# Kernel tuning notes

Measured on AMD Instinct MI355X. Metric: run time of the kernel, lower is better.

The kernel has to match this reference:

```python
import jax, jax.numpy as jnp
import numpy as np

N_NODES = 50000
N_EDGES = 800000


def gat_conv(x, src, dst, ea, W, We, a_s, a_d, a_e, b, n_nodes):
    """PyG GATConv with edge_dim, add_self_loops=True, fill_value='mean', concat=True."""
    H, C = a_s.shape
    dt = x.dtype
    # self-loop edge_attr = mean of incoming edge attrs per destination node
    deg = jax.ops.segment_sum(jnp.ones((src.shape[0],), dt), dst, num_segments=n_nodes)
    loop_attr = jax.ops.segment_sum(ea, dst, num_segments=n_nodes) / jnp.clip(deg, 1.0)[:, None]
    nodes = jnp.arange(n_nodes, dtype=src.dtype)
    s = jnp.concatenate([src, nodes])
    d = jnp.concatenate([dst, nodes])
    e_attr = jnp.concatenate([ea, loop_attr], axis=0)       # [E2, edge_dim]
    h = (x @ W).reshape(n_nodes, H, C)                       # [N,H,C]
    e = (e_attr @ We).reshape(-1, H, C)                      # [E2,H,C]
    a_src = jnp.einsum('nhc,hc->nh', h, a_s)                 # [N,H]
    a_dst = jnp.einsum('nhc,hc->nh', h, a_d)
    a_edg = jnp.einsum('ehc,hc->eh', e, a_e)                 # [E2,H]
    lg = jax.nn.leaky_relu(a_src[s] + a_dst[d] + a_edg, 0.2)  # [E2,H]
    m = jax.ops.segment_max(lg, d, num_segments=n_nodes)     # every node has a self-loop
    p = jnp.exp(lg - m[d])
    z = jax.ops.segment_sum(p, d, num_segments=n_nodes)
    alpha = p / z[d]                                         # segment softmax over dst
    out = jax.ops.segment_sum(alpha[:, :, None] * h[s], d, num_segments=n_nodes)
    return out.reshape(n_nodes, H * C) + b


def setup_inputs() -> dict:
    key = jax.random.key(0)
    ks = iter(jax.random.split(key, 40))
    sc = 0.05
    inp = {
        'x': jax.random.normal(next(ks), (N_NODES, 128), jnp.float32),
        'edge_index': jax.random.randint(next(ks), (2, N_EDGES), 0, N_NODES, dtype=jnp.int32),
        'edge_attr': jax.random.uniform(next(ks), (N_EDGES, 1), jnp.float32),
        'fa_w': jax.random.normal(next(ks), (128, 128)) * sc, 'fa_b': jnp.zeros((128,)),
        'W1': jax.random.normal(next(ks), (128, 256)) * sc, 'We1': jax.random.normal(next(ks), (1, 256)) * sc,
        'as1': jax.random.normal(next(ks), (4, 64)) * sc, 'ad1': jax.random.normal(next(ks), (4, 64)) * sc,
        'ae1': jax.random.normal(next(ks), (4, 64)) * sc, 'b1': jnp.zeros((256,)),
        'W2': jax.random.normal(next(ks), (256, 256)) * sc, 'We2': jax.random.normal(next(ks), (1, 256)) * sc,
        'as2': jax.random.normal(next(ks), (4, 64)) * sc, 'ad2': jax.random.normal(next(ks), (4, 64)) * sc,
        'ae2': jax.random.normal(next(ks), (4, 64)) * sc, 'b2': jnp.zeros((256,)),
        'W3': jax.random.normal(next(ks), (256, 64)) * sc, 'We3': jax.random.normal(next(ks), (1, 64)) * sc,
        'as3': jax.random.normal(next(ks), (1, 64)) * sc, 'ad3': jax.random.normal(next(ks), (1, 64)) * sc,
        'ae3': jax.random.normal(next(ks), (1, 64)) * sc, 'b3': jnp.zeros((64,)),
        'r1_w': jax.random.normal(next(ks), (128, 256)) * sc, 'r1_b': jnp.zeros((256,)),
        'r2_w': jax.random.normal(next(ks), (256, 256)) * sc, 'r2_b': jnp.zeros((256,)),
        'ffn_w1': jax.random.normal(next(ks), (128, 64)) * sc, 'ffn_b1': jnp.zeros((64,)),
        'ffn_w2': jax.random.normal(next(ks), (64, 64)) * sc, 'ffn_b2': jnp.zeros((64,)),
    }
    return inp


def reference(x, edge_index, edge_attr, fa_w, fa_b,
              W1, We1, as1, ad1, ae1, b1,
              W2, We2, as2, ad2, ae2, b2,
              W3, We3, as3, ad3, ae3, b3,
              r1_w, r1_b, r2_w, r2_b,
              ffn_w1, ffn_b1, ffn_w2, ffn_b2):
    n = x.shape[0]
    src, dst = edge_index[0], edge_index[1]
    # feature attention gate
    x = x * jax.nn.sigmoid(x @ fa_w + fa_b)
    xr1 = x @ r1_w + r1_b
    z1 = gat_conv(x, src, dst, edge_attr, W1, We1, as1, ad1, ae1, b1, n)
    z1 = jax.nn.leaky_relu(z1, 0.01) + xr1          # dropout = identity (eval)
    z2 = gat_conv(z1, src, dst, edge_attr, W2, We2, as2, ad2, ae2, b2, n)
    z2 = jax.nn.leaky_relu(z2, 0.01) + (z1 @ r2_w + r2_b)
    z3 = gat_conv(z2, src, dst, edge_attr, W3, We3, as3, ad3, ae3, b3, n)
    z_self = jax.nn.relu(x @ ffn_w1 + ffn_b1) @ ffn_w2 + ffn_b2
    z3 = jax.nn.leaky_relu(z3, 0.01) + z_self
    return z3
```

## Files before the change

### kernel.cpp

```cpp
#include <hip/hip_runtime.h>
#include <hip/hip_bf16.h>


typedef unsigned short u16;
typedef unsigned int   u32;
typedef __attribute__((ext_vector_type(8))) short short8;
typedef __attribute__((ext_vector_type(4))) float float4v;

typedef const __attribute__((address_space(1))) u32* gptr_t;
typedef __attribute__((address_space(3))) u32* lptr_t;
#define GLOAD_LDS16(g, l) \
    __builtin_amdgcn_global_load_lds((gptr_t)(const void*)(g), (lptr_t)(void*)(l), 16, 0, 0)

static __device__ __forceinline__ u16 f2b(float f) {
    u32 u = __float_as_uint(f);
    u32 r = u + 0x7fffu + ((u >> 16) & 1u);
    return (u16)(r >> 16);
}
static __device__ __forceinline__ float b2f(u16 u) {
    return __uint_as_float(((u32)u) << 16);
}
static __device__ __forceinline__ float lo2f(u32 v) { return __uint_as_float(v << 16); }
static __device__ __forceinline__ float hi2f(u32 v) { return __uint_as_float(v & 0xffff0000u); }
static __device__ __forceinline__ float lrelu02(float x) { return fmaxf(x, 0.2f * x); }

__global__ void prep_mega(const float* __restrict__ x, u16* __restrict__ xb, int n4,
                          const float* s0, const float* s1, const float* s2,
                          const float* s3, const float* s4, const float* s5,
                          const float* s6, const float* s7,
                          u16* d0, u16* d1, u16* d2, u16* d3,
                          u16* d4, u16* d5, u16* d6, u16* d7,
                          const float* We1, const float* ae1,
                          const float* We2, const float* ae2,
                          const float* We3, const float* ae3, float* ce_g,
                          const int* __restrict__ ei,
                          u32* deg, u32* rank, int E) {
    int role = blockIdx.y;
    if (role == 0) {
        int i = blockIdx.x * 256 + threadIdx.x;
        if (i >= n4) return;
        float4 v = ((const float4*)x)[i];
        ushort4 o;
        o.x = f2b(v.x); o.y = f2b(v.y); o.z = f2b(v.z); o.w = f2b(v.w);
        ((ushort4*)xb)[i] = o;
    } else if (role == 2) {
        int e = blockIdx.x * 256 + threadIdx.x;
        if (e >= E) return;
        int d = ei[E + e];
        rank[e] = atomicAdd(&deg[d], 1u);
    } else {
        int wid = blockIdx.x >> 4, sub = blockIdx.x & 15;
        if (wid > 8) return;
        if (wid == 8) {
            if (sub == 0) {
                int t = threadIdx.x;
                if (t < 9) {
                    const float* W; const float* a; int h;
                    if (t < 4)      { W = We1; a = ae1; h = t; }
                    else if (t < 8) { W = We2; a = ae2; h = t - 4; }
                    else            { W = We3; a = ae3; h = 0; }
                    float s = 0.f;
                    for (int c = 0; c < 64; c++) s += W[h * 64 + c] * a[h * 64 + c];
                    ce_g[t] = s;
                }
            }
            return;
        }
        const float* src; u16* dst; int K, N;
        switch (wid) {
            case 0: src = s0; dst = d0; K = 128; N = 128; break;
            case 1: src = s1; dst = d1; K = 128; N = 256; break;
            case 2: src = s2; dst = d2; K = 128; N = 256; break;
            case 3: src = s3; dst = d3; K = 256; N = 256; break;
            case 4: src = s4; dst = d4; K = 256; N = 256; break;
            case 5: src = s5; dst = d5; K = 256; N = 64;  break;
            case 6: src = s6; dst = d6; K = 128; N = 64;  break;
            default: src = s7; dst = d7; K = 64;  N = 64;  break;
        }
        int KN = K * N;
        int nmask = N - 1;
        int nshift = __popc((u32)nmask);
        for (int i = sub * 256 + threadIdx.x; i < KN; i += 16 * 256) {
            int k = i >> nshift, n2 = i & nmask;
            dst[(size_t)n2 * K + k] = f2b(src[i]);
        }
    }
}

__global__ void scan_block_kernel(const u32* __restrict__ deg, int* incl,
                                  int* blocksum, int Nn) {
    __shared__ int sb[256];
    int t = threadIdx.x;
    int n = blockIdx.x * 256 + t;
    int v = (n < Nn) ? (int)deg[n] : 0;
    sb[t] = v;
    __syncthreads();
    for (int off = 1; off < 256; off <<= 1) {
        int x = (t >= off) ? sb[t - off] : 0;
        __syncthreads();
        sb[t] += x;
        __syncthreads();
    }
    if (n < Nn) incl[n] = sb[t];
    if (t == 255) blocksum[blockIdx.x] = sb[255];
}

__global__ void scan_final_kernel(const u32* __restrict__ deg, const int* __restrict__ incl,
                                  const int* __restrict__ blocksum,
                                  int* row_ptr, int Nn) {
    __shared__ int sb[256];
    int t = threadIdx.x;
    int b = blockIdx.x;
    sb[t] = (t < b) ? blocksum[t] : 0;
    __syncthreads();
    for (int off = 128; off > 0; off >>= 1) {
        if (t < off) sb[t] += sb[t + off];
        __syncthreads();
    }
    int base = sb[0];
    int n = b * 256 + t;
    if (n >= Nn) return;
    int d = (int)deg[n];
    int excl = base + incl[n] - d;
    row_ptr[n] = excl;
    if (n == Nn - 1) row_ptr[Nn] = excl + d;
}

__global__ void scatter_kernel(const int* __restrict__ ei, const float* __restrict__ ea,
                               const int* __restrict__ row_ptr, const u32* __restrict__ rank,
                               int2* __restrict__ csr2, int E) {
    int e = blockIdx.x * 256 + threadIdx.x;
    if (e >= E) return;
    int d = ei[E + e];
    int pos = row_ptr[d] + (int)rank[e];
    csr2[pos] = make_int2(ei[e], __float_as_int(ea[e]));
}

template <int EPI, int K>
__global__ __launch_bounds__(256)
void gemm128_kernel(const u16* __restrict__ A, const u16* __restrict__ Bt,
                    const float* __restrict__ bias1, const float* __restrict__ bias2,
                    u16* __restrict__ Cres, u16* __restrict__ Ch, u16* __restrict__ Cmid) {
    __shared__ u16 As[128 * 32];
    __shared__ u16 Bs[128 * 32];
    int t = threadIdx.x;
    int w = t >> 6, lane = t & 63;
    int wm = w & 1, wn = w >> 1;
    int lm = lane & 15, q = lane >> 4;
    int bm = blockIdx.x * 128, bn = blockIdx.y * 128;

    float4v acc[4][4];
#pragma unroll
    for (int i = 0; i < 4; i++)
#pragma unroll
        for (int j = 0; j < 4; j++) acc[i][j] = (float4v){0.f, 0.f, 0.f, 0.f};

    int srow = lane >> 2;
    int scol = (lane & 3) * 8;
    const u16* aG = A + (size_t)(bm + w * 32 + srow) * K + scol;
    const u16* bG = Bt + (size_t)(bn + w * 32 + srow) * K + scol;
    u16* aL0 = &As[(w * 32) * 32];
    u16* aL1 = &As[(w * 32 + 16) * 32];
    u16* bL0 = &Bs[(w * 32) * 32];
    u16* bL1 = &Bs[(w * 32 + 16) * 32];

#pragma unroll
    for (int k0 = 0; k0 < K; k0 += 32) {
        GLOAD_LDS16(aG + k0, aL0);
        GLOAD_LDS16(aG + (size_t)16 * K + k0, aL1);
        GLOAD_LDS16(bG + k0, bL0);
        GLOAD_LDS16(bG + (size_t)16 * K + k0, bL1);
        __syncthreads();

        short8 af[4], bf[4];
#pragma unroll
        for (int i = 0; i < 4; i++)
            af[i] = *(const short8*)&As[(64 * wm + 16 * i + lm) * 32 + q * 8];
#pragma unroll
        for (int j = 0; j < 4; j++)
            bf[j] = *(const short8*)&Bs[(64 * wn + 16 * j + lm) * 32 + q * 8];
#pragma unroll
        for (int i = 0; i < 4; i++)
#pragma unroll
            for (int j = 0; j < 4; j++)
                acc[i][j] = __builtin_amdgcn_mfma_f32_16x16x32_bf16(af[i], bf[j], acc[i][j], 0, 0, 0);
        __syncthreads();
    }

#pragma unroll
    for (int i = 0; i < 4; i++)
#pragma unroll
        for (int j = 0; j < 4; j++) {
            int col = bn + 64 * wn + 16 * j + lm;
#pragma unroll
            for (int r = 0; r < 4; r++) {
                int row = bm + 64 * wm + 16 * i + q * 4 + r;
                float v = acc[i][j][r];
                if (col < 256) {
                    Cres[(size_t)row * 256 + col] = f2b(v + bias1[col]);
                } else if (EPI == 4 || col < 512) {
                    Ch[(size_t)row * 256 + (col - 256)] = f2b(v);
                } else if (col < 576) {
                    Cmid[(size_t)row * 64 + (col - 512)] = f2b(fmaxf(v + bias2[col - 512], 0.f));
                }
            }
        }
}

template <int EPI, int K>
__global__ __launch_bounds__(256)
void gemm_kernel(const u16* __restrict__ A, const u16* __restrict__ Bt,
                 const float* __restrict__ bias, const u16* __restrict__ extraB,
                 u16* __restrict__ Cb, int N) {
#define LDSS 40
    __shared__ u16 As[64 * LDSS];
    __shared__ u16 Bs[64 * LDSS];
    int t = threadIdx.x;
    int bm = blockIdx.x * 64, bn = blockIdx.y * 64;
    int w = t >> 6, lane = t & 63;
    int wm = w & 1, wn = w >> 1;
    int lm = lane & 15, q = lane >> 4;

    float4v acc[2][2];
#pragma unroll
    for (int i = 0; i < 2; i++)
#pragma unroll
        for (int j = 0; j < 2; j++) acc[i][j] = (float4v){0.f, 0.f, 0.f, 0.f};

    int ar = t >> 2;
    int ac = (t & 3) * 8;
    const u16* aPtr = A + (size_t)(bm + ar) * K + ac;
    const u16* bPtr = Bt + (size_t)(bn + ar) * K + ac;

#pragma unroll
    for (int k0 = 0; k0 < K; k0 += 32) {
        uint4 av = *(const uint4*)(aPtr + k0);
        uint4 bv = *(const uint4*)(bPtr + k0);
        *(uint4*)&As[ar * LDSS + ac] = av;
        *(uint4*)&Bs[ar * LDSS + ac] = bv;
        __syncthreads();

        short8 fa0 = *(const short8*)&As[(32 * wm + lm) * LDSS + q * 8];
        short8 fa1 = *(const short8*)&As[(32 * wm + 16 + lm) * LDSS + q * 8];
        short8 fb0 = *(const short8*)&Bs[(32 * wn + lm) * LDSS + q * 8];
        short8 fb1 = *(const short8*)&Bs[(32 * wn + 16 + lm) * LDSS + q * 8];
        acc[0][0] = __builtin_amdgcn_mfma_f32_16x16x32_bf16(fa0, fb0, acc[0][0], 0, 0, 0);
        acc[0][1] = __builtin_amdgcn_mfma_f32_16x16x32_bf16(fa0, fb1, acc[0][1], 0, 0, 0);
        acc[1][0] = __builtin_amdgcn_mfma_f32_16x16x32_bf16(fa1, fb0, acc[1][0], 0, 0, 0);
        acc[1][1] = __builtin_amdgcn_mfma_f32_16x16x32_bf16(fa1, fb1, acc[1][1], 0, 0, 0);
        __syncthreads();
    }

#pragma unroll
    for (int i = 0; i < 2; i++)
#pragma unroll
        for (int j = 0; j < 2; j++) {
            int col = bn + 32 * wn + 16 * j + lm;
            float bval = (EPI >= 1) ? bias[col] : 0.f;
#pragma unroll
            for (int r = 0; r < 4; r++) {
                int row = bm + 32 * wm + 16 * i + q * 4 + r;
                float v = acc[i][j][r] + bval;
                if (EPI == 3) {
                    float xv = b2f(extraB[(size_t)row * N + col]);
                    v = xv / (1.f + __expf(-v));
                }
                Cb[(size_t)row * N + col] = f2b(v);
            }
        }
}

__global__ __launch_bounds__(256)
void att4_kernel(const uint2* __restrict__ hb2, const float* __restrict__ a_s,
                 const float* __restrict__ a_d, float* att_s, float* att_d, int Nn) {
    int wv = threadIdx.x >> 6;
    int n = blockIdx.x * 4 + wv;
    if (n >= Nn) return;
    int lane = threadIdx.x & 63;
    float4 as4 = *(const float4*)&a_s[lane * 4];
    float4 ad4 = *(const float4*)&a_d[lane * 4];
    uint2 v = hb2[(size_t)n * 64 + lane];
    float c0 = lo2f(v.x), c1 = hi2f(v.x), c2 = lo2f(v.y), c3 = hi2f(v.y);
    float ps = c0 * as4.x + c1 * as4.y + c2 * as4.z + c3 * as4.w;
    float pd = c0 * ad4.x + c1 * ad4.y + c2 * ad4.z + c3 * ad4.w;
#pragma unroll
    for (int off = 8; off > 0; off >>= 1) {
        ps += __shfl_down(ps, off);
        pd += __shfl_down(pd, off);
    }
    if ((lane & 15) == 0) {
        att_s[n * 4 + (lane >> 4)] = ps;
        att_d[n * 4 + (lane >> 4)] = pd;
    }
}

__global__ __launch_bounds__(256)
void att1_kernel(const u32* __restrict__ hb, const float* __restrict__ a_s,
                 const float* __restrict__ a_d, float* att_s, float* att_d, int Nn) {
    int wv = threadIdx.x >> 6;
    int n = blockIdx.x * 4 + wv;
    if (n >= Nn) return;
    int lane = threadIdx.x & 63;
    int cl = lane & 31;
    float2 as2 = *(const float2*)&a_s[cl * 2];
    float2 ad2 = *(const float2*)&a_d[cl * 2];
    u32 v = hb[(u32)n * 32u + cl];
    float c0 = lo2f(v), c1 = hi2f(v);
    float ps = c0 * as2.x + c1 * as2.y;
    float pd = c0 * ad2.x + c1 * ad2.y;
    if (lane >= 32) { ps = 0.f; pd = 0.f; }
#pragma unroll
    for (int off = 16; off > 0; off >>= 1) {
        ps += __shfl_down(ps, off);
        pd += __shfl_down(pd, off);
    }
    if (lane == 0) {
        att_s[n] = ps;
        att_d[n] = pd;
    }
}

__global__ __launch_bounds__(256)
void agg4_kernel(const uint2* __restrict__ hb2,
                 const float* __restrict__ att_s, const float* __restrict__ att_d,
                 const int* __restrict__ row_ptr, const int2* __restrict__ csr2,
                 const float* __restrict__ ce_g, const float* __restrict__ bias,
                 const uint2* __restrict__ resid2, u16* __restrict__ outb, int Nn) {
    int wv = __builtin_amdgcn_readfirstlane(threadIdx.x >> 6);
    int n = blockIdx.x * 4 + wv;
    if (n >= Nn) return;
    int lane = threadIdx.x & 63;
    int hh = lane >> 4;

    float ce = ce_g[hh];
    float adn = att_d[n * 4 + hh];
    float asn = att_s[n * 4 + hh];
    uint2 sv = hb2[(size_t)n * 64 + lane];
    float z = 0.f, qsum = 0.f;
    float aA0 = 0.f, aA1 = 0.f, aA2 = 0.f, aA3 = 0.f;
    float aB0 = 0.f, aB1 = 0.f, aB2 = 0.f, aB3 = 0.f;

    int e0 = row_ptr[n], e1 = row_ptr[n + 1];
    for (int base = e0; base < e1; base += 64) {
        int cnt = min(64, e1 - base);
        int2 cc = csr2[base + min(lane, cnt - 1)];
        int vsrc = cc.x;
        float vea = __int_as_float(cc.y);
        int i = 0;
        for (; i + 4 <= cnt; i += 4) {
            int sA = __shfl(vsrc, i),     sB = __shfl(vsrc, i + 1);
            int sC = __shfl(vsrc, i + 2), sD = __shfl(vsrc, i + 3);
            float qA = __shfl(vea, i),     qB = __shfl(vea, i + 1);
            float qC = __shfl(vea, i + 2), qD = __shfl(vea, i + 3);
            float gA = att_s[(u32)sA * 4u + hh], gB = att_s[(u32)sB * 4u + hh];
            float gC = att_s[(u32)sC * 4u + hh], gD = att_s[(u32)sD * 4u + hh];
            uint2 vA = hb2[(u32)sA * 64u + lane], vB = hb2[(u32)sB * 64u + lane];
            uint2 vC = hb2[(u32)sC * 64u + lane], vD = hb2[(u32)sD * 64u + lane];
            float pA = __expf(lrelu02(gA + adn + qA * ce));
            float pB = __expf(lrelu02(gB + adn + qB * ce));
            float pC = __expf(lrelu02(gC + adn + qC * ce));
            float pD = __expf(lrelu02(gD + adn + qD * ce));
            qsum += (qA + qB) + (qC + qD);
            z += (pA + pB) + (pC + pD);
            aA0 = fmaf(pA, lo2f(vA.x), aA0); aA1 = fmaf(pA, hi2f(vA.x), aA1);
            aA2 = fmaf(pA, lo2f(vA.y), aA2); aA3 = fmaf(pA, hi2f(vA.y), aA3);
            aB0 = fmaf(pB, lo2f(vB.x), aB0); aB1 = fmaf(pB, hi2f(vB.x), aB1);
            aB2 = fmaf(pB, lo2f(vB.y), aB2); aB3 = fmaf(pB, hi2f(vB.y), aB3);
            aA0 = fmaf(pC, lo2f(vC.x), aA0); aA1 = fmaf(pC, hi2f(vC.x), aA1);
            aA2 = fmaf(pC, lo2f(vC.y), aA2); aA3 = fmaf(pC, hi2f(vC.y), aA3);
            aB0 = fmaf(pD, lo2f(vD.x), aB0); aB1 = fmaf(pD, hi2f(vD.x), aB1);
            aB2 = fmaf(pD, lo2f(vD.y), aB2); aB3 = fmaf(pD, hi2f(vD.y), aB3);
        }
        for (; i < cnt; i++) {
            int s = __shfl(vsrc, i);
            float q = __shfl(vea, i);
            float g = att_s[(u32)s * 4u + hh];
            uint2 v = hb2[(u32)s * 64u + lane];
            float p = __expf(lrelu02(g + adn + q * ce));
            qsum += q;
            z += p;
            aA0 = fmaf(p, lo2f(v.x), aA0); aA1 = fmaf(p, hi2f(v.x), aA1);
            aA2 = fmaf(p, lo2f(v.y), aA2); aA3 = fmaf(p, hi2f(v.y), aA3);
        }
    }
    float la = qsum / (float)max(e1 - e0, 1);
    float ps = __expf(lrelu02(asn + adn + la * ce));
    z += ps;
    float a0 = aA0 + aB0 + ps * lo2f(sv.x);
    float a1 = aA1 + aB1 + ps * hi2f(sv.x);
    float a2 = aA2 + aB2 + ps * lo2f(sv.y);
    float a3 = aA3 + aB3 + ps * hi2f(sv.y);

    float inv = 1.f / z;
    int c0 = lane * 4;
    float4 bv = *(const float4*)&bias[c0];
    uint2 rr = resid2[(size_t)n * 64 + lane];
    float o0 = fmaf(a0, inv, bv.x);
    float o1 = fmaf(a1, inv, bv.y);
    float o2 = fmaf(a2, inv, bv.z);
    float o3 = fmaf(a3, inv, bv.w);
    o0 = fmaxf(o0, 0.01f * o0) + lo2f(rr.x);
    o1 = fmaxf(o1, 0.01f * o1) + hi2f(rr.x);
    o2 = fmaxf(o2, 0.01f * o2) + lo2f(rr.y);
    o3 = fmaxf(o3, 0.01f * o3) + hi2f(rr.y);
    uint2 packed;
    packed.x = ((u32)f2b(o0)) | (((u32)f2b(o1)) << 16);
    packed.y = ((u32)f2b(o2)) | (((u32)f2b(o3)) << 16);
    ((uint2*)outb)[(size_t)n * 64 + lane] = packed;
}

__global__ __launch_bounds__(256)
void agg1_kernel(const uint2* __restrict__ hb2,
                 const float* __restrict__ att_s, const float* __restrict__ att_d,
                 const int* __restrict__ row_ptr, const int2* __restrict__ csr2,
                 const float* __restrict__ ce_g, const float* __restrict__ bias,
                 const uint2* __restrict__ zs2, float* __restrict__ outf, int Nn) {
    int wv = __builtin_amdgcn_readfirstlane(threadIdx.x >> 6);
    int n = blockIdx.x * 4 + wv;
    if (n >= Nn) return;
    int lane = threadIdx.x & 63;
    int qtr = lane >> 4;
    int cl = lane & 15;

    float ce = ce_g[8];
    float adn = att_d[n];
    float asn = att_s[n];
    uint2 sv = hb2[(u32)n * 16u + cl];
    float z = 0.f, qsum = 0.f;
    float a0 = 0.f, a1 = 0.f, a2 = 0.f, a3 = 0.f;

    int e0 = row_ptr[n], e1 = row_ptr[n + 1];
    for (int base = e0; base < e1; base += 64) {
        int cnt = min(64, e1 - base);
        int2 cc = csr2[base + min(lane, cnt - 1)];
        int vsrc = cc.x;
        float vea = __int_as_float(cc.y);
        for (int i = 0; i < cnt; i += 4) {
            int idx = min(i + qtr, cnt - 1);
            int s = __shfl(vsrc, idx);
            float q = __shfl(vea, idx);
            bool act = (i + qtr < cnt);
            float p = __expf(lrelu02(att_s[s] + adn + q * ce));
            p = act ? p : 0.f;
            q = act ? q : 0.f;
            uint2 v = hb2[(u32)s * 16u + cl];
            z += p;
            qsum += q;
            a0 = fmaf(p, lo2f(v.x), a0);
            a1 = fmaf(p, hi2f(v.x), a1);
            a2 = fmaf(p, lo2f(v.y), a2);
            a3 = fmaf(p, hi2f(v.y), a3);
        }
    }
    z += __shfl_xor(z, 16);       z += __shfl_xor(z, 32);
    qsum += __shfl_xor(qsum, 16); qsum += __shfl_xor(qsum, 32);
    a0 += __shfl_xor(a0, 16);     a0 += __shfl_xor(a0, 32);
    a1 += __shfl_xor(a1, 16);     a1 += __shfl_xor(a1, 32);
    a2 += __shfl_xor(a2, 16);     a2 += __shfl_xor(a2, 32);
    a3 += __shfl_xor(a3, 16);     a3 += __shfl_xor(a3, 32);

    float la = qsum / (float)max(e1 - e0, 1);
    float ps = __expf(lrelu02(asn + adn + la * ce));
    z += ps;
    a0 += ps * lo2f(sv.x);
    a1 += ps * hi2f(sv.x);
    a2 += ps * lo2f(sv.y);
    a3 += ps * hi2f(sv.y);

    if (lane < 16) {
        float inv = 1.f / z;
        int c0 = cl * 4;
        float4 bv = *(const float4*)&bias[c0];
        uint2 zz = zs2[(u32)n * 16u + cl];
        float o0 = fmaf(a0, inv, bv.x);
        float o1 = fmaf(a1, inv, bv.y);
        float o2 = fmaf(a2, inv, bv.z);
        float o3 = fmaf(a3, inv, bv.w);
        o0 = fmaxf(o0, 0.01f * o0) + lo2f(zz.x);
        o1 = fmaxf(o1, 0.01f * o1) + hi2f(zz.x);
        o2 = fmaxf(o2, 0.01f * o2) + lo2f(zz.y);
        o3 = fmaxf(o3, 0.01f * o3) + hi2f(zz.y);
        *(float4*)&outf[(size_t)n * 64 + c0] = make_float4(o0, o1, o2, o3);
    }
}

extern "C" void kernel_launch(void* const* d_in, const int* in_sizes, int n_in,
                              void* d_out, int out_size, void* d_ws, size_t ws_size,
                              hipStream_t stream) {
    const float* x    = (const float*)d_in[0];
    const int*   ei   = (const int*)d_in[1];
    const float* ea   = (const float*)d_in[2];
    const float* fa_w = (const float*)d_in[3];
    const float* fa_b = (const float*)d_in[4];
    const float* W1   = (const float*)d_in[5];
    const float* We1  = (const float*)d_in[6];
    const float* as1  = (const float*)d_in[7];
    const float* ad1  = (const float*)d_in[8];
    const float* ae1  = (const float*)d_in[9];
    const float* b1   = (const float*)d_in[10];
    const float* W2   = (const float*)d_in[11];
    const float* We2  = (const float*)d_in[12];
    const float* as2  = (const float*)d_in[13];
    const float* ad2  = (const float*)d_in[14];
    const float* ae2  = (const float*)d_in[15];
    const float* b2   = (const float*)d_in[16];
    const float* W3   = (const float*)d_in[17];
    const float* We3  = (const float*)d_in[18];
    const float* as3  = (const float*)d_in[19];
    const float* ad3  = (const float*)d_in[20];
    const float* ae3  = (const float*)d_in[21];
    const float* b3   = (const float*)d_in[22];
    const float* r1_w = (const float*)d_in[23];
    const float* r1_b = (const float*)d_in[24];
    const float* r2_w = (const float*)d_in[25];
    const float* r2_b = (const float*)d_in[26];
    const float* fw1  = (const float*)d_in[27];
    const float* fb1  = (const float*)d_in[28];
    const float* fw2  = (const float*)d_in[29];
    const float* fb2  = (const float*)d_in[30];

    const int Nn = in_sizes[0] / 128;
    const int E  = in_sizes[1] / 2;

    char* ws = (char*)d_ws;
    size_t off = 0;
    auto alloc = [&](size_t bytes) -> char* {
        char* p = ws + off;
        off += (bytes + 255) & ~((size_t)255);
        return p;
    };
    u32*   deg      = (u32*)alloc((size_t)Nn * 4);
    u32*   rank     = (u32*)alloc((size_t)E * 4);
    int*   incl     = (int*)alloc((size_t)Nn * 4);
    int*   row_ptr  = (int*)alloc((size_t)(Nn + 1) * 4);
    int*   blocksum = (int*)alloc(1024);
    float* att_s    = (float*)alloc((size_t)Nn * 16);
    float* att_d    = (float*)alloc((size_t)Nn * 16);
    int2*  csr2     = (int2*)alloc((size_t)E * 8);
    float* ce_g     = (float*)alloc(64);
    u16* xbf   = (u16*)alloc((size_t)(Nn + 128) * 128 * 2);
    u16* xg_bf = (u16*)alloc((size_t)(Nn + 128) * 128 * 2);
    u16* h_bf  = (u16*)alloc((size_t)(Nn + 128) * 256 * 2);
    u16* z_bf  = (u16*)alloc((size_t)(Nn + 128) * 256 * 2);
    u16* mid_bf = (u16*)alloc((size_t)(Nn + 128) * 64 * 2);
    u16* h3_bf  = (u16*)alloc((size_t)(Nn + 128) * 64 * 2);
    u16* wt_fa = (u16*)alloc(16384 * 2);
    u16* wt_c1 = (u16*)alloc((size_t)640 * 128 * 2);
    u16* wt_c2 = (u16*)alloc((size_t)512 * 256 * 2);
    u16* wt_W3 = (u16*)alloc(16384 * 2);
    u16* wt_f2 = (u16*)alloc(4096 * 2);
    u16* residB = (u16*)alloc((size_t)(Nn + 128) * 256 * 2);
    u16* zself  = (u16*)alloc((size_t)(Nn + 128) * 64 * 2);

    hipMemsetAsync(deg, 0, (size_t)Nn * 4, stream);

    int eb = (E + 255) / 256;
    int nb = (Nn + 255) / 256;
    int n4 = Nn * 128 / 4;
    int xb4 = (n4 + 255) / 256;

    prep_mega<<<dim3(max(xb4, eb), 3), 256, 0, stream>>>(
        x, xbf, n4,
        fa_w, r1_w, W1, r2_w, W2, W3, fw1, fw2,
        wt_fa, wt_c1, wt_c1 + (size_t)256 * 128, wt_c2, wt_c2 + (size_t)256 * 256,
        wt_W3, wt_c1 + (size_t)512 * 128, wt_f2, We1, ae1, We2, ae2, We3, ae3, ce_g,
        ei, deg, rank, E);
    scan_block_kernel<<<nb, 256, 0, stream>>>(deg, incl, blocksum, Nn);
    scan_final_kernel<<<nb, 256, 0, stream>>>(deg, incl, blocksum, row_ptr, Nn);
    scatter_kernel<<<eb, 256, 0, stream>>>(ei, ea, row_ptr, rank, csr2, E);

    int mb  = (Nn + 63) / 64;
    int mb1 = (Nn + 127) / 128;
    int ab  = (Nn + 3) / 4;

    gemm_kernel<3, 128><<<dim3(mb, 2), 256, 0, stream>>>(xbf, wt_fa, fa_b, xbf, xg_bf, 128);
    gemm128_kernel<6, 128><<<dim3(mb1, 5), 256, 0, stream>>>(xg_bf, wt_c1, r1_b, fb1,
                                                             residB, h_bf, mid_bf);
    att4_kernel<<<ab, 256, 0, stream>>>((const uint2*)h_bf, as1, ad1, att_s, att_d, Nn);
    agg4_kernel<<<ab, 256, 0, stream>>>((const uint2*)h_bf, att_s, att_d, row_ptr, csr2,
                                        ce_g, b1, (const uint2*)residB, z_bf, Nn);
    gemm128_kernel<4, 256><<<dim3(mb1, 4), 256, 0, stream>>>(z_bf, wt_c2, r2_b, nullptr,
                                                             residB, h_bf, nullptr);
    att4_kernel<<<ab, 256, 0, stream>>>((const uint2*)h_bf, as2, ad2, att_s, att_d, Nn);
    agg4_kernel<<<ab, 256, 0, stream>>>((const uint2*)h_bf, att_s, att_d, row_ptr, csr2,
                                        ce_g + 4, b2, (const uint2*)residB, z_bf, Nn);
    gemm_kernel<1, 64><<<dim3(mb, 1), 256, 0, stream>>>(mid_bf, wt_f2, fb2, nullptr, zself, 64);
    gemm_kernel<0, 256><<<dim3(mb, 1), 256, 0, stream>>>(z_bf, wt_W3, nullptr, nullptr, h3_bf, 64);
    att1_kernel<<<ab, 256, 0, stream>>>((const u32*)h3_bf, as3, ad3, att_s, att_d, Nn);
    agg1_kernel<<<ab, 256, 0, stream>>>((const uint2*)h3_bf, att_s, att_d, row_ptr, csr2,
                                        ce_g, b3, (const uint2*)zself, (float*)d_out, Nn);
}
```

Before: 494.8 us.

## Co-schedule CSR build with feature-gate and first combined GEMM

Moves the degree-counting atomics out of the prep kernel and into a merged launch alongside the feature-attention gate GEMM, using interleaved block roles. The CSR scatter is likewise merged into the first layer's combined GEMM launch, with one role in six doing a grid-stride scatter. This is meant to overlap the memory-bound graph preprocessing with compute-bound GEMMs and to drop a separate kernel launch. The trade-off is that the scatter and atomic roles use fewer blocks with grid-stride loops, which could lengthen the critical path if they finish after the GEMM blocks.

```diff
diff --git a/kernel.cpp b/kernel.cpp
--- a/kernel.cpp
+++ b/kernel.cpp
@@ -32,9 +32,7 @@
                           u16* d4, u16* d5, u16* d6, u16* d7,
                           const float* We1, const float* ae1,
                           const float* We2, const float* ae2,
-                          const float* We3, const float* ae3, float* ce_g,
-                          const int* __restrict__ ei,
-                          u32* deg, u32* rank, int E) {
+                          const float* We3, const float* ae3, float* ce_g) {
     int role = blockIdx.y;
     if (role == 0) {
         int i = blockIdx.x * 256 + threadIdx.x;
@@ -43,11 +41,6 @@
         ushort4 o;
         o.x = f2b(v.x); o.y = f2b(v.y); o.z = f2b(v.z); o.w = f2b(v.w);
         ((ushort4*)xb)[i] = o;
-    } else if (role == 2) {
-        int e = blockIdx.x * 256 + threadIdx.x;
-        if (e >= E) return;
-        int d = ei[E + e];
-        rank[e] = atomicAdd(&deg[d], 1u);
     } else {
         int wid = blockIdx.x >> 4, sub = blockIdx.x & 15;
         if (wid > 8) return;
@@ -126,28 +119,101 @@
     if (n == Nn - 1) row_ptr[Nn] = excl + d;
 }
 
-__global__ void scatter_kernel(const int* __restrict__ ei, const float* __restrict__ ea,
-                               const int* __restrict__ row_ptr, const u32* __restrict__ rank,
-                               int2* __restrict__ csr2, int E) {
-    int e = blockIdx.x * 256 + threadIdx.x;
-    if (e >= E) return;
-    int d = ei[E + e];
-    int pos = row_ptr[d] + (int)rank[e];
-    csr2[pos] = make_int2(ei[e], __float_as_int(ea[e]));
-}
-
-template <int EPI, int K>
+#define LDSS 40
 __global__ __launch_bounds__(256)
-void gemm128_kernel(const u16* __restrict__ A, const u16* __restrict__ Bt,
-                    const float* __restrict__ bias1, const float* __restrict__ bias2,
-                    u16* __restrict__ Cres, u16* __restrict__ Ch, u16* __restrict__ Cmid) {
+void fa_atomic_kernel(const u16* __restrict__ A, const u16* __restrict__ Bt,
+                      const float* __restrict__ bias, const u16* __restrict__ extraB,
+                      u16* __restrict__ Cb,
+                      const int* __restrict__ ei, u32* deg, u32* rank, int E, int nx) {
+    int gid = blockIdx.x;
+    int role = gid % 3;
+    int idx = gid / 3;
+    if (role == 2) {
+        for (int e = idx * 256 + threadIdx.x; e < E; e += nx * 256)
+            rank[e] = atomicAdd(&deg[ei[E + e]], 1u);
+        return;
+    }
+    __shared__ u16 As[64 * LDSS];
+    __shared__ u16 Bs[64 * LDSS];
+    const int K = 128, N = 128;
+    int t = threadIdx.x;
+    int bm = idx * 64, bn = role * 64;
+    int w = t >> 6, lane = t & 63;
+    int wm = w & 1, wn = w >> 1;
+    int lm = lane & 15, q = lane >> 4;
+
+    float4v acc[2][2];
+#pragma unroll
+    for (int i = 0; i < 2; i++)
+#pragma unroll
+        for (int j = 0; j < 2; j++) acc[i][j] = (float4v){0.f, 0.f, 0.f, 0.f};
+
+    int ar = t >> 2;
+    int ac = (t & 3) * 8;
+    const u16* aPtr = A + (size_t)(bm + ar) * K + ac;
+    const u16* bPtr = Bt + (size_t)(bn + ar) * K + ac;
+
+#pragma unroll
+    for (int k0 = 0; k0 < K; k0 += 32) {
+        uint4 av = *(const uint4*)(aPtr + k0);
+        uint4 bv = *(const uint4*)(bPtr + k0);
+        *(uint4*)&As[ar * LDSS + ac] = av;
+        *(uint4*)&Bs[ar * LDSS + ac] = bv;
+        __syncthreads();
+
+        short8 fa0 = *(const short8*)&As[(32 * wm + lm) * LDSS + q * 8];
+        short8 fa1 = *(const short8*)&As[(32 * wm + 16 + lm) * LDSS + q * 8];
+        short8 fb0 = *(const short8*)&Bs[(32 * wn + lm) * LDSS + q * 8];
+        short8 fb1 = *(const short8*)&Bs[(32 * wn + 16 + lm) * LDSS + q * 8];
+        acc[0][0] = __builtin_amdgcn_mfma_f32_16x16x32_bf16(fa0, fb0, acc[0][0], 0, 0, 0);
+        acc[0][1] = __builtin_amdgcn_mfma_f32_16x16x32_bf16(fa0, fb1, acc[0][1], 0, 0, 0);
+        acc[1][0] = __builtin_amdgcn_mfma_f32_16x16x32_bf16(fa1, fb0, acc[1][0], 0, 0, 0);
+        acc[1][1] = __builtin_amdgcn_mfma_f32_16x16x32_bf16(fa1, fb1, acc[1][1], 0, 0, 0);
+        __syncthreads();
+    }
+
+#pragma unroll
+    for (int i = 0; i < 2; i++)
+#pragma unroll
+        for (int j = 0; j < 2; j++) {
+            int col = bn + 32 * wn + 16 * j + lm;
+            float bval = bias[col];
+#pragma unroll
+            for (int r = 0; r < 4; r++) {
+                int row = bm + 32 * wm + 16 * i + q * 4 + r;
+                float v = acc[i][j][r] + bval;
+                float xv = b2f(extraB[(size_t)row * N + col]);
+                v = xv / (1.f + __expf(-v));
+                Cb[(size_t)row * N + col] = f2b(v);
+            }
+        }
+}
+
+__global__ __launch_bounds__(256)
+void c1_scatter_kernel(const u16* __restrict__ A, const u16* __restrict__ Bt,
+                       const float* __restrict__ bias1, const float* __restrict__ bias2,
+                       u16* __restrict__ Cres, u16* __restrict__ Ch, u16* __restrict__ Cmid,
+                       const int* __restrict__ ei, const float* __restrict__ ea,
+                       const int* __restrict__ row_ptr, const u32* __restrict__ rank,
+                       int2* __restrict__ csr2, int E, int nx) {
+    int gid = blockIdx.x;
+    int role = gid % 6;
+    int idx = gid / 6;
+    if (role == 5) {
+        for (int e = idx * 256 + threadIdx.x; e < E; e += nx * 256) {
+            int d = ei[E + e];
+            csr2[row_ptr[d] + (int)rank[e]] = make_int2(ei[e], __float_as_int(ea[e]));
+        }
+        return;
+    }
     __shared__ u16 As[128 * 32];
     __shared__ u16 Bs[128 * 32];
+    const int K = 128;
     int t = threadIdx.x;
     int w = t >> 6, lane = t & 63;
     int wm = w & 1, wn = w >> 1;
     int lm = lane & 15, q = lane >> 4;
-    int bm = blockIdx.x * 128, bn = blockIdx.y * 128;
+    int bm = idx * 128, bn = role * 128;
 
     float4v acc[4][4];
 #pragma unroll
@@ -198,7 +264,7 @@
                 float v = acc[i][j][r];
                 if (col < 256) {
                     Cres[(size_t)row * 256 + col] = f2b(v + bias1[col]);
-                } else if (EPI == 4 || col < 512) {
+                } else if (col < 512) {
                     Ch[(size_t)row * 256 + (col - 256)] = f2b(v);
                 } else if (col < 576) {
                     Cmid[(size_t)row * 64 + (col - 512)] = f2b(fmaxf(v + bias2[col - 512], 0.f));
@@ -207,12 +273,79 @@
         }
 }
 
+template <int K>
+__global__ __launch_bounds__(256)
+void gemm128_kernel(const u16* __restrict__ A, const u16* __restrict__ Bt,
+                    const float* __restrict__ bias1,
+                    u16* __restrict__ Cres, u16* __restrict__ Ch) {
+    __shared__ u16 As[128 * 32];
+    __shared__ u16 Bs[128 * 32];
+    int t = threadIdx.x;
+    int w = t >> 6, lane = t & 63;
+    int wm = w & 1, wn = w >> 1;
+    int lm = lane & 15, q = lane >> 4;
+    int bm = blockIdx.x * 128, bn = blockIdx.y * 128;
+
+    float4v acc[4][4];
+#pragma unroll
+    for (int i = 0; i < 4; i++)
+#pragma unroll
+        for (int j = 0; j < 4; j++) acc[i][j] = (float4v){0.f, 0.f, 0.f, 0.f};
+
+    int srow = lane >> 2;
+    int scol = (lane & 3) * 8;
+    const u16* aG = A + (size_t)(bm + w * 32 + srow) * K + scol;
+    const u16* bG = Bt + (size_t)(bn + w * 32 + srow) * K + scol;
+    u16* aL0 = &As[(w * 32) * 32];
+    u16* aL1 = &As[(w * 32 + 16) * 32];
+    u16* bL0 = &Bs[(w * 32) * 32];
+    u16* bL1 = &Bs[(w * 32 + 16) * 32];
+
+#pragma unroll
+    for (int k0 = 0; k0 < K; k0 += 32) {
+        GLOAD_LDS16(aG + k0, aL0);
+        GLOAD_LDS16(aG + (size_t)16 * K + k0, aL1);
+        GLOAD_LDS16(bG + k0, bL0);
+        GLOAD_LDS16(bG + (size_t)16 * K + k0, bL1);
+        __syncthreads();
+
+        short8 af[4], bf[4];
+#pragma unroll
+        for (int i = 0; i < 4; i++)
+            af[i] = *(const short8*)&As[(64 * wm + 16 * i + lm) * 32 + q * 8];
+#pragma unroll
+        for (int j = 0; j < 4; j++)
+            bf[j] = *(const short8*)&Bs[(64 * wn + 16 * j + lm) * 32 + q * 8];
+#pragma unroll
+        for (int i = 0; i < 4; i++)
+#pragma unroll
+            for (int j = 0; j < 4; j++)
+                acc[i][j] = __builtin_amdgcn_mfma_f32_16x16x32_bf16(af[i], bf[j], acc[i][j], 0, 0, 0);
+        __syncthreads();
+    }
+
+#pragma unroll
+    for (int i = 0; i < 4; i++)
+#pragma unroll
+        for (int j = 0; j < 4; j++) {
+            int col = bn + 64 * wn + 16 * j + lm;
+#pragma unroll
+            for (int r = 0; r < 4; r++) {
+                int row = bm + 64 * wm + 16 * i + q * 4 + r;
+                float v = acc[i][j][r];
+                if (col < 256) {
+                    Cres[(size_t)row * 256 + col] = f2b(v + bias1[col]);
+                } else {
+                    Ch[(size_t)row * 256 + (col - 256)] = f2b(v);
+                }
+            }
+        }
+}
+
 template <int EPI, int K>
 __global__ __launch_bounds__(256)
 void gemm_kernel(const u16* __restrict__ A, const u16* __restrict__ Bt,
-                 const float* __restrict__ bias, const u16* __restrict__ extraB,
-                 u16* __restrict__ Cb, int N) {
-#define LDSS 40
+                 const float* __restrict__ bias, u16* __restrict__ Cb, int N) {
     __shared__ u16 As[64 * LDSS];
     __shared__ u16 Bs[64 * LDSS];
     int t = threadIdx.x;
@@ -261,10 +394,6 @@
             for (int r = 0; r < 4; r++) {
                 int row = bm + 32 * wm + 16 * i + q * 4 + r;
                 float v = acc[i][j][r] + bval;
-                if (EPI == 3) {
-                    float xv = b2f(extraB[(size_t)row * N + col]);
-                    v = xv / (1.f + __expf(-v));
-                }
                 Cb[(size_t)row * N + col] = f2b(v);
             }
         }
@@ -554,38 +683,36 @@
 
     hipMemsetAsync(deg, 0, (size_t)Nn * 4, stream);
 
-    int eb = (E + 255) / 256;
     int nb = (Nn + 255) / 256;
     int n4 = Nn * 128 / 4;
     int xb4 = (n4 + 255) / 256;
 
-    prep_mega<<<dim3(max(xb4, eb), 3), 256, 0, stream>>>(
+    prep_mega<<<dim3(xb4, 2), 256, 0, stream>>>(
         x, xbf, n4,
         fa_w, r1_w, W1, r2_w, W2, W3, fw1, fw2,
         wt_fa, wt_c1, wt_c1 + (size_t)256 * 128, wt_c2, wt_c2 + (size_t)256 * 256,
-        wt_W3, wt_c1 + (size_t)512 * 128, wt_f2, We1, ae1, We2, ae2, We3, ae3, ce_g,
-        ei, deg, rank, E);
-    scan_block_kernel<<<nb, 256, 0, stream>>>(deg, incl, blocksum, Nn);
-    scan_final_kernel<<<nb, 256, 0, stream>>>(deg, incl, blocksum, row_ptr, Nn);
-    scatter_kernel<<<eb, 256, 0, stream>>>(ei, ea, row_ptr, rank, csr2, E);
+        wt_W3, wt_c1 + (size_t)512 * 128, wt_f2, We1, ae1, We2, ae2, We3, ae3, ce_g);
 
     int mb  = (Nn + 63) / 64;
     int mb1 = (Nn + 127) / 128;
     int ab  = (Nn + 3) / 4;
 
-    gemm_kernel<3, 128><<<dim3(mb, 2), 256, 0, stream>>>(xbf, wt_fa, fa_b, xbf, xg_bf, 128);
-    gemm128_kernel<6, 128><<<dim3(mb1, 5), 256, 0, stream>>>(xg_bf, wt_c1, r1_b, fb1,
-                                                             residB, h_bf, mid_bf);
+    fa_atomic_kernel<<<mb * 3, 256, 0, stream>>>(xbf, wt_fa, fa_b, xbf, xg_bf,
+                                                 ei, deg, rank, E, mb);
+    scan_block_kernel<<<nb, 256, 0, stream>>>(deg, incl, blocksum, Nn);
+    scan_final_kernel<<<nb, 256, 0, stream>>>(deg, incl, blocksum, row_ptr, Nn);
+    c1_scatter_kernel<<<mb1 * 6, 256, 0, stream>>>(xg_bf, wt_c1, r1_b, fb1,
+                                                   residB, h_bf, mid_bf,
+                                                   ei, ea, row_ptr, rank, csr2, E, mb1);
     att4_kernel<<<ab, 256, 0, stream>>>((const uint2*)h_bf, as1, ad1, att_s, att_d, Nn);
     agg4_kernel<<<ab, 256, 0, stream>>>((const uint2*)h_bf, att_s, att_d, row_ptr, csr2,
                                         ce_g, b1, (const uint2*)residB, z_bf, Nn);
-    gemm128_kernel<4, 256><<<dim3(mb1, 4), 256, 0, stream>>>(z_bf, wt_c2, r2_b, nullptr,
-                                                             residB, h_bf, nullptr);
+    gemm128_kernel<256><<<dim3(mb1, 4), 256, 0, stream>>>(z_bf, wt_c2, r2_b, residB, h_bf);
     att4_kernel<<<ab, 256, 0, stream>>>((const uint2*)h_bf, as2, ad2, att_s, att_d, Nn);
     agg4_kernel<<<ab, 256, 0, stream>>>((const uint2*)h_bf, att_s, att_d, row_ptr, csr2,
                                         ce_g + 4, b2, (const uint2*)residB, z_bf, Nn);
-    gemm_kernel<1, 64><<<dim3(mb, 1), 256, 0, stream>>>(mid_bf, wt_f2, fb2, nullptr, zself, 64);
-    gemm_kernel<0, 256><<<dim3(mb, 1), 256, 0, stream>>>(z_bf, wt_W3, nullptr, nullptr, h3_bf, 64);
+    gemm_kernel<1, 64><<<dim3(mb, 1), 256, 0, stream>>>(mid_bf, wt_f2, fb2, zself, 64);
+    gemm_kernel<0, 256><<<dim3(mb, 1), 256, 0, stream>>>(z_bf, wt_W3, nullptr, h3_bf, 64);
     att1_kernel<<<ab, 256, 0, stream>>>((const u32*)h3_bf, as3, ad3, att_s, att_d, Nn);
     agg1_kernel<<<ab, 256, 0, stream>>>((const uint2*)h3_bf, att_s, att_d, row_ptr, csr2,
                                         ce_g, b3, (const uint2*)zself, (float*)d_out, Nn);
```

Result: no change. 487.3 us (-1.5%).
